# Kernel optimization log

Hardware: AMD Instinct MI355X
Metric: run time of the kernel (lower is better)

The kernel has to match this reference:

```python
import jax, jax.numpy as jnp
import numpy as np

D = 512; H = 8; HD = D // H; L = 6; QD = 16; MAXLEN = 1000

def _pos_encoding(max_len, d):
    pos = jnp.arange(max_len, dtype=jnp.float32)[:, None]
    div = jnp.exp(jnp.arange(0, d, 2, dtype=jnp.float32) * (-np.log(10000.0) / d))
    pe = jnp.zeros((max_len, d), jnp.float32)
    pe = pe.at[:, 0::2].set(jnp.sin(pos * div))
    pe = pe.at[:, 1::2].set(jnp.cos(pos * div))
    return pe

def _quantum(x, W, b, qwr, qwi, sg, em, mb):
    # QuantumInspiredLayer: classical tanh branch + quantum branch fused by sigmoid gate
    classical = jnp.tanh(x @ W + b)
    qs = x @ sg                          # (B,S,QD) real superposition amplitudes
    ev_r = qs @ qwr                      # complex evolution, real/imag parts kept separate
    ev_i = qs @ qwi
    en_r = ev_r @ em                     # entanglement (real matrix)
    en_i = ev_i @ em
    probs = en_r ** 2 + en_i ** 2        # |entangled|^2, (B,S,QD)
    qout = probs @ mb                    # measurement, (B,S,D)
    fw = jax.nn.sigmoid(jnp.mean(probs, axis=-1, keepdims=True))  # (B,S,1)
    return fw * qout + (1.0 - fw) * classical, probs

def _layer(x, p):
    (Wq, bq, Wk, bk, Wv, bv, Wo, bo,
     qW, qb, qr, qi, qsg, qem, qmb,
     kW, kb, kr, ki, ksg, kem, kmb, g, beta) = p
    B, S, _ = x.shape
    Q = x @ Wq + bq
    K = x @ Wk + bk
    Vv = x @ Wv + bv
    Qq, qp = _quantum(x, qW, qb, qr, qi, qsg, qem, qmb)
    Kq, kp = _quantum(x, kW, kb, kr, ki, ksg, kem, kmb)
    Qf = (0.7 * Q + 0.3 * Qq).reshape(B, S, H, HD).transpose(0, 2, 1, 3)  # (B,H,S,hd)
    Kf = (0.7 * K + 0.3 * Kq).reshape(B, S, H, HD).transpose(0, 2, 1, 3)
    Vh = Vv.reshape(B, S, H, HD).transpose(0, 2, 1, 3)
    scores = jnp.einsum('bhid,bhjd->bhij', Qf, Kf) / np.sqrt(HD).astype(np.float32)
    interf = jnp.einsum('biq,bjq->bij', qp, kp)   # quantum interference term (B,S,S)
    scores = scores + 0.1 * interf[:, None]       # broadcast over heads
    attn = jax.nn.softmax(scores, axis=-1)        # dropout=eval mode (identity)
    ctx = jnp.einsum('bhij,bhjd->bhid', attn, Vh).transpose(0, 2, 1, 3).reshape(B, S, D)
    y = ctx @ Wo + bo + x                         # residual, then LayerNorm
    mu = jnp.mean(y, axis=-1, keepdims=True)
    var = jnp.mean((y - mu) ** 2, axis=-1, keepdims=True)
    y = (y - mu) / jnp.sqrt(var + 1e-5) * g + beta
    return y, attn

def setup_inputs() -> dict:
    key = jax.random.key(0)
    ks = iter(jax.random.split(key, 64))
    def rn(shape, s=0.02):
        return (jax.random.normal(next(ks), shape) * s).astype(jnp.float32)
    B, S, V = 4, 512, 32000
    inp = {
        'text_input': jax.random.randint(next(ks), (B, S), 0, V),
        'visual_input': rn((B, 2048), 1.0),
        'temporal_input': rn((B, 64), 1.0),
        'embed': rn((V, D)),
        'Wvis': rn((2048, D)), 'bvis': jnp.zeros((D,), jnp.float32),
        'Wtemp': rn((64, D)), 'btemp': jnp.zeros((D,), jnp.float32),
        'Wq': rn((L, D, D)), 'bq': jnp.zeros((L, D), jnp.float32),
        'Wk': rn((L, D, D)), 'bk': jnp.zeros((L, D), jnp.float32),
        'Wv': rn((L, D, D)), 'bv': jnp.zeros((L, D), jnp.float32),
        'Wo': rn((L, D, D)), 'bo': jnp.zeros((L, D), jnp.float32),
        'qW': rn((L, D, D)), 'qb': jnp.zeros((L, D), jnp.float32),
        'q_qwr': rn((L, QD, QD), 0.05), 'q_qwi': rn((L, QD, QD), 0.05),
        'q_sg': rn((L, D, QD), 0.05), 'q_em': rn((L, QD, QD), 0.05), 'q_mb': rn((L, QD, D), 0.05),
        'kW': rn((L, D, D)), 'kb': jnp.zeros((L, D), jnp.float32),
        'k_qwr': rn((L, QD, QD), 0.05), 'k_qwi': rn((L, QD, QD), 0.05),
        'k_sg': rn((L, D, QD), 0.05), 'k_em': rn((L, QD, QD), 0.05), 'k_mb': rn((L, QD, D), 0.05),
        'ln_g': jnp.ones((L, D), jnp.float32), 'ln_b': jnp.zeros((L, D), jnp.float32),
        'Ws': rn((D, 64)), 'bs_': jnp.zeros((64,), jnp.float32),
        'Wd': rn((D, 5)), 'bd': jnp.zeros((5,), jnp.float32),
        'We': rn((D, 1)), 'be': jnp.zeros((1,), jnp.float32),
    }
    return inp

def reference(text_input, visual_input, temporal_input, embed, Wvis, bvis, Wtemp, btemp,
              Wq, bq, Wk, bk, Wv, bv, Wo, bo,
              qW, qb, q_qwr, q_qwi, q_sg, q_em, q_mb,
              kW, kb, k_qwr, k_qwi, k_sg, k_em, k_mb,
              ln_g, ln_b, Ws, bs_, Wd, bd, We, be):
    B, S = text_input.shape
    x = (embed[text_input]
         + (visual_input @ Wvis + bvis)[:, None, :]
         + (temporal_input @ Wtemp + btemp)[:, None, :])
    x = x + _pos_encoding(MAXLEN, D)[None, :S, :]
    attns = []
    for l in range(L):
        p = (Wq[l], bq[l], Wk[l], bk[l], Wv[l], bv[l], Wo[l], bo[l],
             qW[l], qb[l], q_qwr[l], q_qwi[l], q_sg[l], q_em[l], q_mb[l],
             kW[l], kb[l], k_qwr[l], k_qwi[l], k_sg[l], k_em[l], k_mb[l],
             ln_g[l], ln_b[l])
        x, a = _layer(x, p)
        attns.append(a)
    pooled = jnp.mean(x, axis=1)  # no attention_mask -> simple mean pool
    skill = jax.nn.sigmoid(pooled @ Ws + bs_)
    diff = jax.nn.softmax(pooled @ Wd + bd, axis=-1)
    eng = jax.nn.sigmoid(pooled @ We + be)
    return skill, diff, eng, x, jnp.stack(attns)
```

## Files before the change

### kernel.cpp

```cpp
#include <hip/hip_runtime.h>
#include <hip/hip_bf16.h>

typedef __attribute__((ext_vector_type(4))) float f32x4;
typedef __attribute__((ext_vector_type(8))) short s16x8;

__device__ __forceinline__ unsigned short f2b(float f) {
  unsigned int u = __float_as_uint(f);
  unsigned int r = (u + 0x7FFFu + ((u >> 16) & 1u)) >> 16;
  return (unsigned short)r;
}
__device__ __forceinline__ float b2f(unsigned short h) {
  return __uint_as_float(((unsigned int)h) << 16);
}
__device__ __forceinline__ void gload16(const void* g, void* l) {
  __builtin_amdgcn_global_load_lds(
      (const __attribute__((address_space(1))) void*)g,
      (__attribute__((address_space(3))) void*)l, 16, 0, 0);
}

enum { MODE_F32 = 0, MODE_VT = 1, MODE_Y = 2 };
struct OutSpec { void* ptr; int mode; };
struct Outs5 { OutSpec o[5]; };
struct Ptr6 { const float* p[6]; };

template<int BM, int BN, int WGM, int WGN>
__global__ __launch_bounds__(256) void gemm_nt(
    const unsigned short* __restrict__ A, int lda, long long strideA,
    const unsigned short* __restrict__ Bm, int ldb, long long strideB,
    const float* __restrict__ biasBase, int biasStride, int perZ,
    Outs5 outs, const float* __restrict__ resid, int K)
{
  constexpr int BK = 32;
  constexpr int WM = BM / WGM, WN = BN / WGN;
  constexpr int WR = WM / 16, WC = WN / 16;
  constexpr int CHA = BM * BK / 8;
  constexpr int CHB = BN * BK / 8;
  __shared__ unsigned short lds_a[2][BM * BK];
  __shared__ unsigned short lds_b[2][BN * BK];
  const int z = blockIdx.z;
  const int tid = threadIdx.x;
  const int wave = tid >> 6, lane = tid & 63;
  const int l16 = lane & 15, lhi = lane >> 4;
  const int wm = (wave / WGN) * WM, wn = (wave % WGN) * WN;
  const int m0 = blockIdx.x * BM, n0 = blockIdx.y * BN;
  const unsigned short* Ap = A + (long long)z * strideA;
  const unsigned short* Bp = Bm + (long long)z * strideB;

  auto stage = [&](int buf, int k0) {
#pragma unroll
    for (int p = 0; p < CHA / 256; ++p) {
      int t = p * 256 + tid;
      gload16(Ap + (long long)(m0 + (t >> 2)) * lda + k0 + (t & 3) * 8, &lds_a[buf][t * 8]);
    }
    if constexpr (CHA % 256) {
      if (tid < CHA % 256) {
        int t = (CHA / 256) * 256 + tid;
        gload16(Ap + (long long)(m0 + (t >> 2)) * lda + k0 + (t & 3) * 8, &lds_a[buf][t * 8]);
      }
    }
#pragma unroll
    for (int p = 0; p < CHB / 256; ++p) {
      int t = p * 256 + tid;
      gload16(Bp + (long long)(n0 + (t >> 2)) * ldb + k0 + (t & 3) * 8, &lds_b[buf][t * 8]);
    }
    if constexpr (CHB % 256) {
      if (tid < CHB % 256) {
        int t = (CHB / 256) * 256 + tid;
        gload16(Bp + (long long)(n0 + (t >> 2)) * ldb + k0 + (t & 3) * 8, &lds_b[buf][t * 8]);
      }
    }
  };

  f32x4 acc[WR][WC];
#pragma unroll
  for (int r = 0; r < WR; ++r)
#pragma unroll
    for (int c = 0; c < WC; ++c) { f32x4 zz = {0.f, 0.f, 0.f, 0.f}; acc[r][c] = zz; }

  stage(0, 0);
  __syncthreads();
  int cur = 0;
  for (int k0 = 0; k0 < K; k0 += BK) {
    if (k0 + BK < K) stage(cur ^ 1, k0 + BK);
    s16x8 af[WR], bfv[WC];
#pragma unroll
    for (int r = 0; r < WR; ++r)
      af[r] = *(const s16x8*)&lds_a[cur][(wm + r * 16 + l16) * BK + lhi * 8];
#pragma unroll
    for (int c = 0; c < WC; ++c)
      bfv[c] = *(const s16x8*)&lds_b[cur][(wn + c * 16 + l16) * BK + lhi * 8];
#pragma unroll
    for (int r = 0; r < WR; ++r)
#pragma unroll
      for (int c = 0; c < WC; ++c)
        acc[r][c] = __builtin_amdgcn_mfma_f32_16x16x32_bf16(af[r], bfv[c], acc[r][c], 0, 0, 0);
    __syncthreads();
    cur ^= 1;
  }

  OutSpec spec = perZ ? outs.o[z] : outs.o[0];
  const float* bias = biasBase ? (biasBase + (long long)z * biasStride) : nullptr;
#pragma unroll
  for (int r = 0; r < WR; ++r) {
#pragma unroll
    for (int c = 0; c < WC; ++c) {
      int n = n0 + wn + c * 16 + l16;
      int rb = m0 + wm + r * 16 + lhi * 4;
      float bv = bias ? bias[n] : 0.f;
      float vv[4];
#pragma unroll
      for (int j = 0; j < 4; ++j) vv[j] = acc[r][c][j] + bv;
      if (spec.mode == MODE_F32) {
#pragma unroll
        for (int j = 0; j < 4; ++j)
          ((float*)spec.ptr)[(long long)(rb + j) * 512 + n] = vv[j];
      } else if (spec.mode == MODE_VT) {
        int b = rb >> 9, s = rb & 511;
        ushort4 pk;
        pk.x = f2b(vv[0]); pk.y = f2b(vv[1]); pk.z = f2b(vv[2]); pk.w = f2b(vv[3]);
        *(ushort4*)&((unsigned short*)spec.ptr)[
            (((long long)(b * 8 + (n >> 6))) * 64 + (n & 63)) * 512 + s] = pk;
      } else {
#pragma unroll
        for (int j = 0; j < 4; ++j)
          ((float*)spec.ptr)[(long long)(rb + j) * 512 + n] =
              vv[j] + resid[(long long)(rb + j) * 512 + n];
      }
    }
  }
}

__global__ __launch_bounds__(256, 1) void fused_attn(
    const unsigned short* __restrict__ Qe, const unsigned short* __restrict__ Ke,
    const unsigned short* __restrict__ Vt, float* __restrict__ attn,
    unsigned short* __restrict__ ctx)
{
  __shared__ unsigned short lds[55296];
  const int z = blockIdx.x, rb = blockIdx.y;
  const int m0 = rb * 64;
  const int b = z >> 3, h = z & 7;
  const int tid = threadIdx.x;
  const int w = tid >> 6, lane = tid & 63;
  const int l16 = lane & 15, lhi = lane >> 4;
  const int rx3 = l16 & 3, rx7 = l16 & 7;

#pragma unroll
  for (int p = 0; p < 3; ++p) {
    int t = p * 256 + tid;
    int row = t / 12, c = t % 12;
    gload16(Qe + ((long long)(z * 512 + m0 + row)) * 96 + (c ^ (row & 3)) * 8, &lds[t * 8]);
  }
#pragma unroll
  for (int p = 0; p < 24; ++p) {
    int t = p * 256 + tid;
    int row = t / 12, c = t % 12;
    gload16(Ke + ((long long)(z * 512 + row)) * 96 + (c ^ (row & 3)) * 8, &lds[6144 + t * 8]);
  }
  __syncthreads();

  const unsigned short* Qs = lds;
  const unsigned short* Ks = lds + 6144;
  s16x8 aq[3];
#pragma unroll
  for (int kk = 0; kk < 3; ++kk)
    aq[kk] = *(const s16x8*)&Qs[(w * 16 + l16) * 96 + (kk * 4 + (lhi ^ rx3)) * 8];
  f32x4 acc[32];
#pragma unroll
  for (int c = 0; c < 32; ++c) { f32x4 zz = {0.f, 0.f, 0.f, 0.f}; acc[c] = zz; }
#pragma unroll
  for (int c = 0; c < 32; ++c) {
#pragma unroll
    for (int kk = 0; kk < 3; ++kk) {
      s16x8 bf = *(const s16x8*)&Ks[(c * 16 + l16) * 96 + (kk * 4 + (lhi ^ rx3)) * 8];
      acc[c] = __builtin_amdgcn_mfma_f32_16x16x32_bf16(aq[kk], bf, acc[c], 0, 0, 0);
    }
  }

  float inv[4];
#pragma unroll
  for (int j = 0; j < 4; ++j) {
    float mx = acc[0][j];
#pragma unroll
    for (int c = 1; c < 32; ++c) mx = fmaxf(mx, acc[c][j]);
    mx = fmaxf(mx, __shfl_xor(mx, 1));
    mx = fmaxf(mx, __shfl_xor(mx, 2));
    mx = fmaxf(mx, __shfl_xor(mx, 4));
    mx = fmaxf(mx, __shfl_xor(mx, 8));
    float sum = 0.f;
#pragma unroll
    for (int c = 0; c < 32; ++c) { float e = __expf(acc[c][j] - mx); acc[c][j] = e; sum += e; }
    sum += __shfl_xor(sum, 1);
    sum += __shfl_xor(sum, 2);
    sum += __shfl_xor(sum, 4);
    sum += __shfl_xor(sum, 8);
    inv[j] = 1.f / sum;
  }
  __syncthreads();

#pragma unroll
  for (int p = 0; p < 8; ++p) {
    int t = p * 256 + tid;
    int row = t >> 5, c = t & 31;
    gload16(Vt + (long long)z * 32768 + row * 512 + (c ^ (row & 7)) * 8, &lds[32768 + t * 8]);
  }
  unsigned short* S = lds;
#pragma unroll
  for (int j = 0; j < 4; ++j) {
    int row_l = w * 16 + lhi * 4 + j;
    int rs = row_l & 7;
    unsigned short* srow = S + row_l * 512;
#pragma unroll
    for (int c = 0; c < 32; ++c) {
      float p = acc[c][j] * inv[j];
      int col = c * 16 + l16;
      srow[((col >> 3) ^ rs) * 8 + (col & 7)] = f2b(p);
    }
  }
  __syncthreads();

  {
    float* ap = attn + (long long)z * 262144;
#pragma unroll
    for (int i = 0; i < 16; ++i) {
      int cid = i * 256 + tid;
      int row = cid >> 6, g = cid & 63;
      int rs = row & 7;
      s16x8 v = *(const s16x8*)&S[row * 512 + (g ^ rs) * 8];
      f32x4 o0, o1;
#pragma unroll
      for (int e = 0; e < 4; ++e) { o0[e] = b2f((unsigned short)v[e]); o1[e] = b2f((unsigned short)v[4 + e]); }
      float* dst = ap + (long long)(m0 + row) * 512 + g * 8;
      *(f32x4*)dst = o0;
      *(f32x4*)(dst + 4) = o1;
    }
  }

  const unsigned short* Vl = lds + 32768;
  f32x4 acc2[4];
#pragma unroll
  for (int c2 = 0; c2 < 4; ++c2) { f32x4 zz = {0.f, 0.f, 0.f, 0.f}; acc2[c2] = zz; }
  const int qrow = w * 16 + l16;
#pragma unroll
  for (int kk = 0; kk < 8; ++kk) {
    s16x8 a = *(const s16x8*)&S[qrow * 512 + ((kk * 4 + lhi) ^ rx7) * 8];
#pragma unroll
    for (int c2 = 0; c2 < 4; ++c2) {
      s16x8 bf = *(const s16x8*)&Vl[(c2 * 16 + l16) * 256 + ((kk * 4 + lhi) ^ rx7) * 8];
      acc2[c2] = __builtin_amdgcn_mfma_f32_16x16x32_bf16(a, bf, acc2[c2], 0, 0, 0);
    }
  }
  __syncthreads();
#pragma unroll
  for (int p = 0; p < 8; ++p) {
    int t = p * 256 + tid;
    int row = t >> 5, c = t & 31;
    gload16(Vt + (long long)z * 32768 + row * 512 + 256 + (c ^ (row & 7)) * 8,
            &lds[32768 + t * 8]);
  }
  __syncthreads();
#pragma unroll
  for (int kk = 8; kk < 16; ++kk) {
    s16x8 a = *(const s16x8*)&S[qrow * 512 + ((kk * 4 + lhi) ^ rx7) * 8];
#pragma unroll
    for (int c2 = 0; c2 < 4; ++c2) {
      s16x8 bf = *(const s16x8*)&Vl[(c2 * 16 + l16) * 256 + (((kk - 8) * 4 + lhi) ^ rx7) * 8];
      acc2[c2] = __builtin_amdgcn_mfma_f32_16x16x32_bf16(a, bf, acc2[c2], 0, 0, 0);
    }
  }
#pragma unroll
  for (int c2 = 0; c2 < 4; ++c2) {
#pragma unroll
    for (int j = 0; j < 4; ++j) {
      int row_g = m0 + w * 16 + lhi * 4 + j;
      ctx[((long long)(b * 512 + row_g)) * 512 + h * 64 + c2 * 16 + l16] = f2b(acc2[c2][j]);
    }
  }
}

__global__ __launch_bounds__(256) void wt_k(Ptr6 srcs, unsigned short* __restrict__ wt) {
  __shared__ float tile[32][33];
  int zz = blockIdx.z;
  int l = zz / 6, mat = zz % 6;
  const float* src = srcs.p[mat] + (long long)l * 262144;
  int tx = threadIdx.x, ty = threadIdx.y;
  int n0 = blockIdx.x * 32, k0 = blockIdx.y * 32;
#pragma unroll
  for (int r = 0; r < 4; ++r)
    tile[ty + r * 8][tx] = src[(long long)(k0 + ty + r * 8) * 512 + n0 + tx];
  __syncthreads();
#pragma unroll
  for (int r = 0; r < 4; ++r)
    wt[(long long)zz * 262144 + (long long)(n0 + ty + r * 8) * 512 + k0 + tx] =
        f2b(tile[tx][ty + r * 8]);
}

__global__ __launch_bounds__(256) void prep_k(Ptr6 biases,
    const float* __restrict__ qwr, const float* __restrict__ qwi, const float* __restrict__ qem,
    const float* __restrict__ kwr, const float* __restrict__ kwi, const float* __restrict__ kem,
    float* __restrict__ biasPacked, float* __restrict__ ArAi) {
  int l = blockIdx.x, t = threadIdx.x;
  for (int m = 0; m < 6; ++m)
    for (int d = t; d < 512; d += 256)
      biasPacked[(l * 6 + m) * 512 + d] = biases.p[m][l * 512 + d];
  int i = t >> 4, j = t & 15;
  const float* em0 = qem + l * 256;
  float ar = 0.f, ai = 0.f;
  for (int tt = 0; tt < 16; ++tt) {
    ar += qwr[l * 256 + i * 16 + tt] * em0[tt * 16 + j];
    ai += qwi[l * 256 + i * 16 + tt] * em0[tt * 16 + j];
  }
  ArAi[(l * 4 + 0) * 256 + t] = ar;
  ArAi[(l * 4 + 1) * 256 + t] = ai;
  const float* em1 = kem + l * 256;
  ar = 0.f; ai = 0.f;
  for (int tt = 0; tt < 16; ++tt) {
    ar += kwr[l * 256 + i * 16 + tt] * em1[tt * 16 + j];
    ai += kwi[l * 256 + i * 16 + tt] * em1[tt * 16 + j];
  }
  ArAi[(l * 4 + 2) * 256 + t] = ar;
  ArAi[(l * 4 + 3) * 256 + t] = ai;
}

__global__ __launch_bounds__(512) void vispart_k(const float* __restrict__ vis,
    const float* __restrict__ Wvis, float* __restrict__ part) {
  int b = blockIdx.x, chunk = blockIdx.y, d = threadIdx.x;
  float acc = 0.f;
  for (int k = chunk * 64; k < chunk * 64 + 64; ++k)
    acc += vis[b * 2048 + k] * Wvis[(long long)k * 512 + d];
  part[(b * 32 + chunk) * 512 + d] = acc;
}
__global__ __launch_bounds__(512) void projsum_k(const float* __restrict__ part,
    const float* __restrict__ bvis, const float* __restrict__ temporal,
    const float* __restrict__ Wtemp, const float* __restrict__ btemp, float* __restrict__ proj) {
  int b = blockIdx.x, d = threadIdx.x;
  float acc = bvis[d] + btemp[d];
  for (int c = 0; c < 32; ++c) acc += part[(b * 32 + c) * 512 + d];
  for (int k = 0; k < 64; ++k) acc += temporal[b * 64 + k] * Wtemp[k * 512 + d];
  proj[b * 512 + d] = acc;
}

__global__ __launch_bounds__(512) void embed_k(const int* __restrict__ text,
    const float* __restrict__ emb, const float* __restrict__ proj,
    float* __restrict__ x, unsigned short* __restrict__ xb) {
  int row = blockIdx.x;
  int b = row >> 9, s = row & 511;
  int d = threadIdx.x;
  int tok = text[row];
  float v = emb[(long long)tok * 512 + d] + proj[b * 512 + d];
  float fr = __expf((float)((d >> 1) << 1) * (-9.2103403719761836f / 512.f));
  float ang = (float)s * fr;
  v += (d & 1) ? cosf(ang) : sinf(ang);
  x[(long long)row * 512 + d] = v;
  xb[(long long)row * 512 + d] = f2b(v);
}

__global__ __launch_bounds__(64) void quantum_k(const float* __restrict__ x,
    const float* __restrict__ sg_q, const float* __restrict__ sg_k,
    const float* __restrict__ ArAiL, float* __restrict__ qp, float* __restrict__ kp,
    float* __restrict__ fwq, float* __restrict__ fwk) {
  int row = blockIdx.x, side = blockIdx.y, lane = threadIdx.x;
  const float* sg = side ? sg_k : sg_q;
  const float* Ar = ArAiL + side * 512;
  const float* Ai = Ar + 256;
  float acc[16];
#pragma unroll
  for (int j = 0; j < 16; ++j) acc[j] = 0.f;
  const float* xr = x + (long long)row * 512;
#pragma unroll
  for (int kk = 0; kk < 8; ++kk) {
    float xv = xr[kk * 64 + lane];
    const float* sgr = sg + (kk * 64 + lane) * 16;
#pragma unroll
    for (int j = 0; j < 16; ++j) acc[j] += xv * sgr[j];
  }
#pragma unroll
  for (int s = 32; s; s >>= 1)
#pragma unroll
    for (int j = 0; j < 16; ++j) acc[j] += __shfl_xor(acc[j], s);
  int j = lane & 15;
  float tr = 0.f, ti = 0.f;
#pragma unroll
  for (int t = 0; t < 16; ++t) {
    tr += acc[t] * Ar[t * 16 + j];
    ti += acc[t] * Ai[t * 16 + j];
  }
  float p = tr * tr + ti * ti;
  float ps = p;
#pragma unroll
  for (int s = 1; s < 16; s <<= 1) ps += __shfl_xor(ps, s);
  if (lane < 16) (side ? kp : qp)[row * 16 + lane] = p;
  if (lane == 0) (side ? fwk : fwq)[row] = 1.f / (1.f + __expf(-ps * (1.f / 16.f)));
}

struct FuseP {
  const float* lin; const float* cl; const float* qp; const float* fw;
  const float* mb; unsigned short* ext; float sA, sB;
};
struct Fuse2 { FuseP s[2]; };
__global__ __launch_bounds__(512) void fuse_k(Fuse2 fp) {
  FuseP P = fp.s[blockIdx.y];
  int row = blockIdx.x;
  int b = row >> 9, i = row & 511;
  int d = threadIdx.x;
  const float* qpr = P.qp + row * 16;
  float fwv = P.fw[row];
  float qout = 0.f;
#pragma unroll
  for (int t = 0; t < 16; ++t) qout += qpr[t] * P.mb[t * 512 + d];
  float qq = fwv * qout + (1.f - fwv) * tanhf(P.cl[(long long)row * 512 + d]);
  float val = (0.7f * P.lin[(long long)row * 512 + d] + 0.3f * qq) * P.sA;
  int h = d >> 6, dd = d & 63;
  P.ext[(((long long)(b * 8 + h)) * 512 + i) * 96 + dd] = f2b(val);
  if (d < 128) {
    int h2 = d >> 4, j = d & 15;
    P.ext[(((long long)(b * 8 + h2)) * 512 + i) * 96 + 64 + j] = f2b(P.sB * qpr[j]);
  } else if (d < 256) {
    int t2 = d - 128;
    int h2 = t2 >> 4, j = t2 & 15;
    P.ext[(((long long)(b * 8 + h2)) * 512 + i) * 96 + 80 + j] = 0;
  }
}

__global__ __launch_bounds__(256) void ln_k(const float* __restrict__ y,
    const float* __restrict__ g, const float* __restrict__ be,
    float* __restrict__ xo, unsigned short* __restrict__ xb, float* __restrict__ xo2) {
  int wv = threadIdx.x >> 6, lane = threadIdx.x & 63;
  long long row = (long long)blockIdx.x * 4 + wv;
  const float* yr = y + row * 512 + lane * 8;
  f32x4 a = *(const f32x4*)yr, b = *(const f32x4*)(yr + 4);
  float s = a[0] + a[1] + a[2] + a[3] + b[0] + b[1] + b[2] + b[3];
#pragma unroll
  for (int m = 32; m; m >>= 1) s += __shfl_xor(s, m);
  float mu = s * (1.f / 512.f);
  float d[8], vs = 0.f;
#pragma unroll
  for (int j = 0; j < 4; ++j) { d[j] = a[j] - mu; vs += d[j] * d[j]; }
#pragma unroll
  for (int j = 0; j < 4; ++j) { d[4 + j] = b[j] - mu; vs += d[4 + j] * d[4 + j]; }
#pragma unroll
  for (int m = 32; m; m >>= 1) vs += __shfl_xor(vs, m);
  float rstd = rsqrtf(vs * (1.f / 512.f) + 1e-5f);
  f32x4 g0 = *(const f32x4*)(g + lane * 8), g1 = *(const f32x4*)(g + lane * 8 + 4);
  f32x4 b0 = *(const f32x4*)(be + lane * 8), b1 = *(const f32x4*)(be + lane * 8 + 4);
  f32x4 o0, o1; s16x8 ob;
#pragma unroll
  for (int j = 0; j < 4; ++j) { o0[j] = d[j] * rstd * g0[j] + b0[j]; ob[j] = (short)f2b(o0[j]); }
#pragma unroll
  for (int j = 0; j < 4; ++j) { o1[j] = d[4 + j] * rstd * g1[j] + b1[j]; ob[4 + j] = (short)f2b(o1[j]); }
  float* xr = xo + row * 512 + lane * 8;
  *(f32x4*)xr = o0; *(f32x4*)(xr + 4) = o1;
  *(s16x8*)(xb + row * 512 + lane * 8) = ob;
  if (xo2) {
    float* x2 = xo2 + row * 512 + lane * 8;
    *(f32x4*)x2 = o0; *(f32x4*)(x2 + 4) = o1;
  }
}

__global__ __launch_bounds__(512) void poolpart_k(const float* __restrict__ x,
                                                   float* __restrict__ part) {
  int b = blockIdx.x, ch = blockIdx.y, d = threadIdx.x;
  float s = 0.f;
  for (int r = 0; r < 64; ++r) s += x[((long long)(b * 512 + ch * 64 + r)) * 512 + d];
  part[(b * 8 + ch) * 512 + d] = s;
}
__global__ __launch_bounds__(512) void head_k(const float* __restrict__ part,
    const float* __restrict__ Ws, const float* __restrict__ bs,
    const float* __restrict__ Wd, const float* __restrict__ bd,
    const float* __restrict__ We, const float* __restrict__ be, float* __restrict__ out) {
  __shared__ float pooled[512];
  __shared__ float dl[5];
  int b = blockIdx.x, d = threadIdx.x;
  float s = 0.f;
  for (int t = 0; t < 8; ++t) s += part[(b * 8 + t) * 512 + d];
  pooled[d] = s * (1.f / 512.f);
  __syncthreads();
  {
    int o = d >> 3, sub = d & 7;
    float a = 0.f;
    for (int t = sub; t < 512; t += 8) a += pooled[t] * Ws[t * 64 + o];
    a += __shfl_xor(a, 1); a += __shfl_xor(a, 2); a += __shfl_xor(a, 4);
    if (sub == 0) out[b * 64 + o] = 1.f / (1.f + __expf(-(a + bs[o])));
  }
  if (d < 40) {
    int o = d >> 3, sub = d & 7;
    float a = 0.f;
    for (int t = sub; t < 512; t += 8) a += pooled[t] * Wd[t * 5 + o];
    a += __shfl_xor(a, 1); a += __shfl_xor(a, 2); a += __shfl_xor(a, 4);
    if (sub == 0) dl[o] = a + bd[o];
  } else if (d >= 64 && d < 72) {
    int sub = d & 7;
    float a = 0.f;
    for (int t = sub; t < 512; t += 8) a += pooled[t] * We[t];
    a += __shfl_xor(a, 1); a += __shfl_xor(a, 2); a += __shfl_xor(a, 4);
    if (sub == 0) out[276 + b] = 1.f / (1.f + __expf(-(a + be[0])));
  }
  __syncthreads();
  if (d < 5) {
    float mx = dl[0];
    for (int j = 1; j < 5; ++j) mx = fmaxf(mx, dl[j]);
    float sm = 0.f;
    for (int j = 0; j < 5; ++j) sm += __expf(dl[j] - mx);
    out[256 + b * 5 + d] = __expf(dl[d] - mx) / sm;
  }
}

extern "C" void kernel_launch(void* const* d_in, const int* in_sizes, int n_in,
                              void* d_out, int out_size, void* d_ws, size_t ws_size,
                              hipStream_t stream) {
  (void)in_sizes; (void)n_in; (void)out_size; (void)ws_size;
  const int*   text     = (const int*)  d_in[0];
  const float* visual   = (const float*)d_in[1];
  const float* temporal = (const float*)d_in[2];
  const float* embedw   = (const float*)d_in[3];
  const float* Wvis  = (const float*)d_in[4];  const float* bvis  = (const float*)d_in[5];
  const float* Wtemp = (const float*)d_in[6];  const float* btemp = (const float*)d_in[7];
  const float* Wq = (const float*)d_in[8];   const float* bq = (const float*)d_in[9];
  const float* Wk = (const float*)d_in[10];  const float* bk = (const float*)d_in[11];
  const float* Wv = (const float*)d_in[12];  const float* bv = (const float*)d_in[13];
  const float* Wo = (const float*)d_in[14];  const float* bo = (const float*)d_in[15];
  const float* qW = (const float*)d_in[16];  const float* qb = (const float*)d_in[17];
  const float* q_qwr = (const float*)d_in[18]; const float* q_qwi = (const float*)d_in[19];
  const float* q_sg  = (const float*)d_in[20]; const float* q_em  = (const float*)d_in[21];
  const float* q_mb  = (const float*)d_in[22];
  const float* kW = (const float*)d_in[23];  const float* kb = (const float*)d_in[24];
  const float* k_qwr = (const float*)d_in[25]; const float* k_qwi = (const float*)d_in[26];
  const float* k_sg  = (const float*)d_in[27]; const float* k_em  = (const float*)d_in[28];
  const float* k_mb  = (const float*)d_in[29];
  const float* ln_g = (const float*)d_in[30]; const float* ln_b = (const float*)d_in[31];
  const float* Ws = (const float*)d_in[32];  const float* bs_ = (const float*)d_in[33];
  const float* Wd = (const float*)d_in[34];  const float* bd = (const float*)d_in[35];
  const float* We = (const float*)d_in[36];  const float* be = (const float*)d_in[37];
  float* out = (float*)d_out;

  char* w = (char*)d_ws;
  auto alloc = [&](size_t bytes) {
    char* p = w;
    w += (bytes + 255) & ~(size_t)255;
    return p;
  };
  float* ws_x   = (float*)alloc(2048ll * 512 * 4);
  unsigned short* ws_xb = (unsigned short*)alloc(2048ll * 512 * 2);
  unsigned short* ws_Wt = (unsigned short*)alloc(36ll * 262144 * 2);
  float* ws_bias = (float*)alloc(6ll * 6 * 512 * 4);
  float* ws_ArAi = (float*)alloc(6ll * 1024 * 4);
  float* ws_proj = (float*)alloc(4ll * 512 * 4);
  float* ws_vp   = (float*)alloc(4ll * 32 * 512 * 4);
  float* ws_Q    = (float*)alloc(2048ll * 512 * 4);
  float* ws_K    = (float*)alloc(2048ll * 512 * 4);
  float* ws_Cq   = (float*)alloc(2048ll * 512 * 4);
  float* ws_Ck   = (float*)alloc(2048ll * 512 * 4);
  float* ws_qp   = (float*)alloc(2048ll * 16 * 4);
  float* ws_kp   = (float*)alloc(2048ll * 16 * 4);
  float* ws_fwq  = (float*)alloc(2048ll * 4);
  float* ws_fwk  = (float*)alloc(2048ll * 4);
  unsigned short* ws_Vt   = (unsigned short*)alloc(2048ll * 512 * 2);
  unsigned short* ws_Qext = (unsigned short*)alloc(4ll * 8 * 512 * 96 * 2);
  unsigned short* ws_Kext = (unsigned short*)alloc(4ll * 8 * 512 * 96 * 2);
  unsigned short* ws_ctx  = (unsigned short*)alloc(2048ll * 512 * 2);
  float* ws_y    = (float*)alloc(2048ll * 512 * 4);

  Ptr6 wsrc = {{Wq, Wk, Wv, qW, kW, Wo}};
  wt_k<<<dim3(16, 16, 36), dim3(32, 8), 0, stream>>>(wsrc, ws_Wt);
  Ptr6 bsrc = {{bq, bk, bv, qb, kb, bo}};
  prep_k<<<dim3(6), dim3(256), 0, stream>>>(bsrc, q_qwr, q_qwi, q_em, k_qwr, k_qwi, k_em,
                                            ws_bias, ws_ArAi);
  vispart_k<<<dim3(4, 32), dim3(512), 0, stream>>>(visual, Wvis, ws_vp);
  projsum_k<<<dim3(4), dim3(512), 0, stream>>>(ws_vp, bvis, temporal, Wtemp, btemp, ws_proj);
  embed_k<<<dim3(2048), dim3(512), 0, stream>>>(text, embedw, ws_proj, ws_x, ws_xb);

  const long long ATTN_OFF = 280ll + 1048576ll;
  for (int l = 0; l < 6; ++l) {
    const unsigned short* WtL = ws_Wt + (long long)l * 6 * 262144;
    const float* biasL = ws_bias + (long long)l * 6 * 512;

    Outs5 o5{};
    o5.o[0] = { ws_Q, MODE_F32 };  o5.o[1] = { ws_K, MODE_F32 };
    o5.o[2] = { ws_Vt, MODE_VT };  o5.o[3] = { ws_Cq, MODE_F32 };
    o5.o[4] = { ws_Ck, MODE_F32 };
    gemm_nt<128, 128, 2, 2><<<dim3(16, 4, 5), 256, 0, stream>>>(
        ws_xb, 512, 0ll, WtL, 512, 262144ll, biasL, 512, 1, o5, nullptr, 512);

    quantum_k<<<dim3(2048, 2), 64, 0, stream>>>(ws_x, q_sg + l * 8192, k_sg + l * 8192,
        ws_ArAi + l * 1024, ws_qp, ws_kp, ws_fwq, ws_fwk);

    Fuse2 f2{};
    f2.s[0] = { ws_Q, ws_Cq, ws_qp, ws_fwq, q_mb + l * 8192, ws_Qext, 0.125f, 0.1f };
    f2.s[1] = { ws_K, ws_Ck, ws_kp, ws_fwk, k_mb + l * 8192, ws_Kext, 1.0f, 1.0f };
    fuse_k<<<dim3(2048, 2), dim3(512), 0, stream>>>(f2);

    fused_attn<<<dim3(32, 8), 256, 0, stream>>>(
        ws_Qext, ws_Kext, ws_Vt, out + ATTN_OFF + (long long)l * 8388608, ws_ctx);

    Outs5 oy{};
    oy.o[0] = { ws_y, MODE_Y };
    gemm_nt<64, 64, 2, 2><<<dim3(32, 8, 1), 256, 0, stream>>>(
        ws_ctx, 512, 0ll, WtL + 5 * 262144, 512, 0ll, biasL + 5 * 512, 0, 0, oy, ws_x, 512);

    ln_k<<<dim3(512), dim3(256), 0, stream>>>(ws_y, ln_g + l * 512, ln_b + l * 512,
        ws_x, ws_xb, (l == 5) ? (out + 280) : nullptr);
  }

  poolpart_k<<<dim3(4, 8), dim3(512), 0, stream>>>(ws_x, ws_vp);
  head_k<<<dim3(4), dim3(512), 0, stream>>>(ws_vp, Ws, bs_, Wd, bd, We, be, out);
}
```

Measured before the change: 521.9 us.

## Fuse output projection GEMM with residual LayerNorm and mean-pool partials

Replaces the Wo GEMM, the separate LayerNorm kernel and the pooling kernel with one kernel. Each block computes full 32-row by 512-column output tiles, adds bias and residual into LDS, normalizes rows in place and, on the last layer, writes per-block pooled partial sums. This removes the fp32 y round trip through global memory and two launches per layer. The cost is only 64 blocks on a large GPU, each block loading the whole Wo weight matrix, and heavy LDS use that lowers occupancy.

```diff
diff --git a/kernel.cpp b/kernel.cpp
--- a/kernel.cpp
+++ b/kernel.cpp
@@ -18,7 +18,7 @@
       (__attribute__((address_space(3))) void*)l, 16, 0, 0);
 }
 
-enum { MODE_F32 = 0, MODE_VT = 1, MODE_Y = 2 };
+enum { MODE_F32 = 0, MODE_VT = 1 };
 struct OutSpec { void* ptr; int mode; };
 struct Outs5 { OutSpec o[5]; };
 struct Ptr6 { const float* p[6]; };
@@ -28,7 +28,7 @@
     const unsigned short* __restrict__ A, int lda, long long strideA,
     const unsigned short* __restrict__ Bm, int ldb, long long strideB,
     const float* __restrict__ biasBase, int biasStride, int perZ,
-    Outs5 outs, const float* __restrict__ resid, int K)
+    Outs5 outs, int K)
 {
   constexpr int BK = 32;
   constexpr int WM = BM / WGM, WN = BN / WGN;
@@ -114,19 +114,142 @@
 #pragma unroll
         for (int j = 0; j < 4; ++j)
           ((float*)spec.ptr)[(long long)(rb + j) * 512 + n] = vv[j];
-      } else if (spec.mode == MODE_VT) {
+      } else {
         int b = rb >> 9, s = rb & 511;
         ushort4 pk;
         pk.x = f2b(vv[0]); pk.y = f2b(vv[1]); pk.z = f2b(vv[2]); pk.w = f2b(vv[3]);
         *(ushort4*)&((unsigned short*)spec.ptr)[
             (((long long)(b * 8 + (n >> 6))) * 64 + (n & 63)) * 512 + s] = pk;
-      } else {
-#pragma unroll
-        for (int j = 0; j < 4; ++j)
-          ((float*)spec.ptr)[(long long)(rb + j) * 512 + n] =
-              vv[j] + resid[(long long)(rb + j) * 512 + n];
       }
     }
+  }
+}
+
+__global__ __launch_bounds__(256) void ygemm_ln(
+    const unsigned short* __restrict__ ctx, const unsigned short* __restrict__ WoT,
+    const float* __restrict__ bias, const float* __restrict__ g, const float* __restrict__ be,
+    float* __restrict__ x, unsigned short* __restrict__ xb,
+    float* __restrict__ xo2, float* __restrict__ pool)
+{
+  __shared__ char smem[77824];
+  unsigned short* lds_a = (unsigned short*)smem;
+  unsigned short* lds_b = (unsigned short*)(smem + 4096);
+  float* ylds = (float*)smem;
+  float* wpart = (float*)(smem + 69632);
+  const int tid = threadIdx.x;
+  const int w = tid >> 6, lane = tid & 63;
+  const int l16 = lane & 15, lhi = lane >> 4;
+  const int m0 = blockIdx.x * 32;
+  const int wn = w * 128;
+
+  auto stage = [&](int buf, int k0) {
+    if (tid < 128) {
+      int row = tid >> 2, cg = tid & 3;
+      gload16(ctx + (long long)(m0 + row) * 512 + k0 + cg * 8, lds_a + buf * 1024 + tid * 8);
+    }
+#pragma unroll
+    for (int p = 0; p < 8; ++p) {
+      int t = p * 256 + tid;
+      int row = t >> 2, cg = t & 3;
+      gload16(WoT + (long long)row * 512 + k0 + cg * 8, lds_b + buf * 16384 + t * 8);
+    }
+  };
+
+  f32x4 acc[2][8];
+#pragma unroll
+  for (int r = 0; r < 2; ++r)
+#pragma unroll
+    for (int c = 0; c < 8; ++c) { f32x4 zz = {0.f, 0.f, 0.f, 0.f}; acc[r][c] = zz; }
+
+  stage(0, 0);
+  __syncthreads();
+  int cur = 0;
+  for (int k0 = 0; k0 < 512; k0 += 32) {
+    if (k0 + 32 < 512) stage(cur ^ 1, k0 + 32);
+    s16x8 af[2], bfv[8];
+#pragma unroll
+    for (int r = 0; r < 2; ++r)
+      af[r] = *(const s16x8*)&lds_a[cur * 1024 + (r * 16 + l16) * 32 + lhi * 8];
+#pragma unroll
+    for (int c = 0; c < 8; ++c)
+      bfv[c] = *(const s16x8*)&lds_b[cur * 16384 + (wn + c * 16 + l16) * 32 + lhi * 8];
+#pragma unroll
+    for (int r = 0; r < 2; ++r)
+#pragma unroll
+      for (int c = 0; c < 8; ++c)
+        acc[r][c] = __builtin_amdgcn_mfma_f32_16x16x32_bf16(af[r], bfv[c], acc[r][c], 0, 0, 0);
+    __syncthreads();
+    cur ^= 1;
+  }
+
+#pragma unroll
+  for (int r = 0; r < 2; ++r) {
+#pragma unroll
+    for (int c = 0; c < 8; ++c) {
+      int col = wn + c * 16 + l16;
+      int rb = r * 16 + lhi * 4;
+      float bv = bias[col];
+#pragma unroll
+      for (int j = 0; j < 4; ++j) {
+        int row = rb + j;
+        ylds[row * 520 + col] = acc[r][c][j] + bv + x[(long long)(m0 + row) * 512 + col];
+      }
+    }
+  }
+  __syncthreads();
+
+  f32x4 g0 = *(const f32x4*)(g + lane * 8), g1 = *(const f32x4*)(g + lane * 8 + 4);
+  f32x4 b0 = *(const f32x4*)(be + lane * 8), b1 = *(const f32x4*)(be + lane * 8 + 4);
+  float psum[8];
+#pragma unroll
+  for (int e = 0; e < 8; ++e) psum[e] = 0.f;
+#pragma unroll
+  for (int i = 0; i < 8; ++i) {
+    int row = w + i * 4;
+    const float* yr = ylds + row * 520 + lane * 8;
+    f32x4 a = *(const f32x4*)yr, bq = *(const f32x4*)(yr + 4);
+    float s = a[0] + a[1] + a[2] + a[3] + bq[0] + bq[1] + bq[2] + bq[3];
+#pragma unroll
+    for (int m = 32; m; m >>= 1) s += __shfl_xor(s, m);
+    float mu = s * (1.f / 512.f);
+    float d[8], vs = 0.f;
+#pragma unroll
+    for (int j = 0; j < 4; ++j) { d[j] = a[j] - mu; vs += d[j] * d[j]; }
+#pragma unroll
+    for (int j = 0; j < 4; ++j) { d[4 + j] = bq[j] - mu; vs += d[4 + j] * d[4 + j]; }
+#pragma unroll
+    for (int m = 32; m; m >>= 1) vs += __shfl_xor(vs, m);
+    float rstd = rsqrtf(vs * (1.f / 512.f) + 1e-5f);
+    f32x4 o0, o1; s16x8 ob;
+#pragma unroll
+    for (int j = 0; j < 4; ++j) { o0[j] = d[j] * rstd * g0[j] + b0[j]; ob[j] = (short)f2b(o0[j]); }
+#pragma unroll
+    for (int j = 0; j < 4; ++j) { o1[j] = d[4 + j] * rstd * g1[j] + b1[j]; ob[4 + j] = (short)f2b(o1[j]); }
+    long long gro = (long long)(m0 + row) * 512 + lane * 8;
+    *(f32x4*)(x + gro) = o0; *(f32x4*)(x + gro + 4) = o1;
+    *(s16x8*)(xb + gro) = ob;
+    if (xo2) { *(f32x4*)(xo2 + gro) = o0; *(f32x4*)(xo2 + gro + 4) = o1; }
+    if (pool) {
+#pragma unroll
+      for (int e = 0; e < 4; ++e) { psum[e] += o0[e]; psum[4 + e] += o1[e]; }
+    }
+  }
+  if (pool) {
+    f32x4 p0, p1;
+#pragma unroll
+    for (int e = 0; e < 4; ++e) { p0[e] = psum[e]; p1[e] = psum[4 + e]; }
+    *(f32x4*)(wpart + w * 512 + lane * 8) = p0;
+    *(f32x4*)(wpart + w * 512 + lane * 8 + 4) = p1;
+    __syncthreads();
+    float s0 = 0.f, s1 = 0.f;
+#pragma unroll
+    for (int w2 = 0; w2 < 4; ++w2) {
+      s0 += wpart[w2 * 512 + tid];
+      s1 += wpart[w2 * 512 + 256 + tid];
+    }
+    long long po = (long long)((m0 >> 9) * 16 + (blockIdx.x & 15)) * 512;
+    pool[po + tid] = s0;
+    pool[po + 256 + tid] = s1;
   }
 }
 
@@ -223,13 +346,13 @@
 #pragma unroll
     for (int i = 0; i < 16; ++i) {
       int cid = i * 256 + tid;
-      int row = cid >> 6, g = cid & 63;
+      int row = cid >> 6, gch = cid & 63;
       int rs = row & 7;
-      s16x8 v = *(const s16x8*)&S[row * 512 + (g ^ rs) * 8];
+      s16x8 v = *(const s16x8*)&S[row * 512 + (gch ^ rs) * 8];
       f32x4 o0, o1;
 #pragma unroll
       for (int e = 0; e < 4; ++e) { o0[e] = b2f((unsigned short)v[e]); o1[e] = b2f((unsigned short)v[4 + e]); }
-      float* dst = ap + (long long)(m0 + row) * 512 + g * 8;
+      float* dst = ap + (long long)(m0 + row) * 512 + gch * 8;
       *(f32x4*)dst = o0;
       *(f32x4*)(dst + 4) = o1;
     }
@@ -421,48 +544,6 @@
   }
 }
 
-__global__ __launch_bounds__(256) void ln_k(const float* __restrict__ y,
-    const float* __restrict__ g, const float* __restrict__ be,
-    float* __restrict__ xo, unsigned short* __restrict__ xb, float* __restrict__ xo2) {
-  int wv = threadIdx.x >> 6, lane = threadIdx.x & 63;
-  long long row = (long long)blockIdx.x * 4 + wv;
-  const float* yr = y + row * 512 + lane * 8;
-  f32x4 a = *(const f32x4*)yr, b = *(const f32x4*)(yr + 4);
-  float s = a[0] + a[1] + a[2] + a[3] + b[0] + b[1] + b[2] + b[3];
-#pragma unroll
-  for (int m = 32; m; m >>= 1) s += __shfl_xor(s, m);
-  float mu = s * (1.f / 512.f);
-  float d[8], vs = 0.f;
-#pragma unroll
-  for (int j = 0; j < 4; ++j) { d[j] = a[j] - mu; vs += d[j] * d[j]; }
-#pragma unroll
-  for (int j = 0; j < 4; ++j) { d[4 + j] = b[j] - mu; vs += d[4 + j] * d[4 + j]; }
-#pragma unroll
-  for (int m = 32; m; m >>= 1) vs += __shfl_xor(vs, m);
-  float rstd = rsqrtf(vs * (1.f / 512.f) + 1e-5f);
-  f32x4 g0 = *(const f32x4*)(g + lane * 8), g1 = *(const f32x4*)(g + lane * 8 + 4);
-  f32x4 b0 = *(const f32x4*)(be + lane * 8), b1 = *(const f32x4*)(be + lane * 8 + 4);
-  f32x4 o0, o1; s16x8 ob;
-#pragma unroll
-  for (int j = 0; j < 4; ++j) { o0[j] = d[j] * rstd * g0[j] + b0[j]; ob[j] = (short)f2b(o0[j]); }
-#pragma unroll
-  for (int j = 0; j < 4; ++j) { o1[j] = d[4 + j] * rstd * g1[j] + b1[j]; ob[4 + j] = (short)f2b(o1[j]); }
-  float* xr = xo + row * 512 + lane * 8;
-  *(f32x4*)xr = o0; *(f32x4*)(xr + 4) = o1;
-  *(s16x8*)(xb + row * 512 + lane * 8) = ob;
-  if (xo2) {
-    float* x2 = xo2 + row * 512 + lane * 8;
-    *(f32x4*)x2 = o0; *(f32x4*)(x2 + 4) = o1;
-  }
-}
-
-__global__ __launch_bounds__(512) void poolpart_k(const float* __restrict__ x,
-                                                   float* __restrict__ part) {
-  int b = blockIdx.x, ch = blockIdx.y, d = threadIdx.x;
-  float s = 0.f;
-  for (int r = 0; r < 64; ++r) s += x[((long long)(b * 512 + ch * 64 + r)) * 512 + d];
-  part[(b * 8 + ch) * 512 + d] = s;
-}
 __global__ __launch_bounds__(512) void head_k(const float* __restrict__ part,
     const float* __restrict__ Ws, const float* __restrict__ bs,
     const float* __restrict__ Wd, const float* __restrict__ bd,
@@ -471,7 +552,7 @@
   __shared__ float dl[5];
   int b = blockIdx.x, d = threadIdx.x;
   float s = 0.f;
-  for (int t = 0; t < 8; ++t) s += part[(b * 8 + t) * 512 + d];
+  for (int t = 0; t < 16; ++t) s += part[(b * 16 + t) * 512 + d];
   pooled[d] = s * (1.f / 512.f);
   __syncthreads();
   {
@@ -557,7 +638,6 @@
   unsigned short* ws_Qext = (unsigned short*)alloc(4ll * 8 * 512 * 96 * 2);
   unsigned short* ws_Kext = (unsigned short*)alloc(4ll * 8 * 512 * 96 * 2);
   unsigned short* ws_ctx  = (unsigned short*)alloc(2048ll * 512 * 2);
-  float* ws_y    = (float*)alloc(2048ll * 512 * 4);
 
   Ptr6 wsrc = {{Wq, Wk, Wv, qW, kW, Wo}};
   wt_k<<<dim3(16, 16, 36), dim3(32, 8), 0, stream>>>(wsrc, ws_Wt);
@@ -578,7 +658,7 @@
     o5.o[2] = { ws_Vt, MODE_VT };  o5.o[3] = { ws_Cq, MODE_F32 };
     o5.o[4] = { ws_Ck, MODE_F32 };
     gemm_nt<128, 128, 2, 2><<<dim3(16, 4, 5), 256, 0, stream>>>(
-        ws_xb, 512, 0ll, WtL, 512, 262144ll, biasL, 512, 1, o5, nullptr, 512);
+        ws_xb, 512, 0ll, WtL, 512, 262144ll, biasL, 512, 1, o5, 512);
 
     quantum_k<<<dim3(2048, 2), 64, 0, stream>>>(ws_x, q_sg + l * 8192, k_sg + l * 8192,
         ws_ArAi + l * 1024, ws_qp, ws_kp, ws_fwq, ws_fwk);
@@ -591,15 +671,11 @@
     fused_attn<<<dim3(32, 8), 256, 0, stream>>>(
         ws_Qext, ws_Kext, ws_Vt, out + ATTN_OFF + (long long)l * 8388608, ws_ctx);
 
-    Outs5 oy{};
-    oy.o[0] = { ws_y, MODE_Y };
-    gemm_nt<64, 64, 2, 2><<<dim3(32, 8, 1), 256, 0, stream>>>(
-        ws_ctx, 512, 0ll, WtL + 5 * 262144, 512, 0ll, biasL + 5 * 512, 0, 0, oy, ws_x, 512);
-
-    ln_k<<<dim3(512), dim3(256), 0, stream>>>(ws_y, ln_g + l * 512, ln_b + l * 512,
-        ws_x, ws_xb, (l == 5) ? (out + 280) : nullptr);
-  }
-
-  poolpart_k<<<dim3(4, 8), dim3(512), 0, stream>>>(ws_x, ws_vp);
+    ygemm_ln<<<dim3(64), dim3(256), 0, stream>>>(
+        ws_ctx, WtL + 5 * 262144, biasL + 5 * 512,
+        ln_g + l * 512, ln_b + l * 512, ws_x, ws_xb,
+        (l == 5) ? (out + 280) : nullptr, (l == 5) ? ws_vp : nullptr);
+  }
+
   head_k<<<dim3(4), dim3(512), 0, stream>>>(ws_vp, Ws, bs_, Wd, bd, We, be, out);
 }
```

Result: slower. 541.8 us (+3.8%).

## Fuse QKV and quantum GEMMs with gating epilogue into one kernel

Applied to the files above, without the earlier changes.

Replaces the five-output projection GEMM plus separate fuse kernel with a single kernel. Each block computes the linear and classical-branch GEMMs together, runs the quantum measurement matmul on MFMA, and writes the bf16 Q/K extended tensors and V transpose directly, which removes the fp32 Q/K/Cq/Ck intermediates and their global round trips. Attention-probability output is also written straight from registers instead of being staged through LDS and re-read, dropping a barrier. In exchange the new GEMM uses smaller tiles with no LDS swizzle, converts probs to bf16 for the measurement product, and writes the ext tensors with scattered stores.

```diff
diff --git a/kernel.cpp b/kernel.cpp
--- a/kernel.cpp
+++ b/kernel.cpp
@@ -130,6 +130,165 @@
   }
 }
 
+__global__ __launch_bounds__(256) void qkv_fuse(
+    const unsigned short* __restrict__ xb, const unsigned short* __restrict__ Wt,
+    const float* __restrict__ biasP,
+    const float* __restrict__ qp, const float* __restrict__ kp,
+    const float* __restrict__ fwq, const float* __restrict__ fwk,
+    const unsigned short* __restrict__ mbT,
+    unsigned short* __restrict__ Qext, unsigned short* __restrict__ Kext,
+    unsigned short* __restrict__ Vt)
+{
+  __shared__ unsigned short lds[2][8192];
+  const int z = blockIdx.z;
+  const int tid = threadIdx.x;
+  const int wave = tid >> 6, lane = tid & 63;
+  const int l16 = lane & 15, lhi = lane >> 4;
+  const int wm = (wave >> 1) * 64, wn = (wave & 1) * 32;
+  const int m0 = blockIdx.x * 128, n0 = blockIdx.y * 64;
+  const int mat1 = z;
+  const unsigned short* B1p = Wt + (long long)mat1 * 262144;
+  const unsigned short* B2p = Wt + (long long)(z + 3) * 262144;
+
+  auto stage = [&](int buf, int k0) {
+#pragma unroll
+    for (int p = 0; p < 2; ++p) {
+      int t = p * 256 + tid;
+      gload16(xb + (long long)(m0 + (t >> 2)) * 512 + k0 + (t & 3) * 8, &lds[buf][t * 8]);
+    }
+    {
+      int row = tid >> 2, cg = tid & 3;
+      gload16(B1p + (long long)(n0 + row) * 512 + k0 + cg * 8, &lds[buf][4096 + tid * 8]);
+      if (z < 2)
+        gload16(B2p + (long long)(n0 + row) * 512 + k0 + cg * 8, &lds[buf][6144 + tid * 8]);
+    }
+  };
+
+  f32x4 acc1[4][2], acc2[4][2];
+#pragma unroll
+  for (int r = 0; r < 4; ++r)
+#pragma unroll
+    for (int c = 0; c < 2; ++c) {
+      f32x4 zz = {0.f, 0.f, 0.f, 0.f};
+      acc1[r][c] = zz; acc2[r][c] = zz;
+    }
+
+  stage(0, 0);
+  __syncthreads();
+  int cur = 0;
+  for (int k0 = 0; k0 < 512; k0 += 32) {
+    if (k0 + 32 < 512) stage(cur ^ 1, k0 + 32);
+    s16x8 af[4], b1f[2], b2f[2];
+#pragma unroll
+    for (int r = 0; r < 4; ++r)
+      af[r] = *(const s16x8*)&lds[cur][(wm + r * 16 + l16) * 32 + lhi * 8];
+#pragma unroll
+    for (int c = 0; c < 2; ++c) {
+      b1f[c] = *(const s16x8*)&lds[cur][4096 + (wn + c * 16 + l16) * 32 + lhi * 8];
+      b2f[c] = *(const s16x8*)&lds[cur][6144 + (wn + c * 16 + l16) * 32 + lhi * 8];
+    }
+#pragma unroll
+    for (int r = 0; r < 4; ++r)
+#pragma unroll
+      for (int c = 0; c < 2; ++c)
+        acc1[r][c] = __builtin_amdgcn_mfma_f32_16x16x32_bf16(af[r], b1f[c], acc1[r][c], 0, 0, 0);
+    if (z < 2) {
+#pragma unroll
+      for (int r = 0; r < 4; ++r)
+#pragma unroll
+        for (int c = 0; c < 2; ++c)
+          acc2[r][c] = __builtin_amdgcn_mfma_f32_16x16x32_bf16(af[r], b2f[c], acc2[r][c], 0, 0, 0);
+    }
+    __syncthreads();
+    cur ^= 1;
+  }
+
+  const float* bias1 = biasP + mat1 * 512;
+  if (z == 2) {
+#pragma unroll
+    for (int r = 0; r < 4; ++r)
+#pragma unroll
+      for (int c = 0; c < 2; ++c) {
+        int n = n0 + wn + c * 16 + l16;
+        int rb = m0 + wm + r * 16 + lhi * 4;
+        float bv = bias1[n];
+        int bb = rb >> 9, s = rb & 511;
+        ushort4 pk;
+        pk.x = f2b(acc1[r][c][0] + bv); pk.y = f2b(acc1[r][c][1] + bv);
+        pk.z = f2b(acc1[r][c][2] + bv); pk.w = f2b(acc1[r][c][3] + bv);
+        *(ushort4*)&Vt[(((long long)(bb * 8 + (n >> 6))) * 64 + (n & 63)) * 512 + s] = pk;
+      }
+    return;
+  }
+
+  const float* probs = z ? kp : qp;
+  const float* fw    = z ? fwk : fwq;
+  unsigned short* ext = z ? Kext : Qext;
+  const unsigned short* mbs = mbT + z * 16384;
+  const float* bias2 = biasP + (z + 3) * 512;
+  const float sA = z ? 1.0f : 0.125f;
+  const float sB = z ? 1.0f : 0.1f;
+
+  s16x8 pf[4];
+#pragma unroll
+  for (int r = 0; r < 4; ++r) {
+    s16x8 v = {0, 0, 0, 0, 0, 0, 0, 0};
+    if (lhi < 2) {
+      const float* pr = probs + (m0 + wm + r * 16 + l16) * 16 + lhi * 8;
+#pragma unroll
+      for (int e = 0; e < 8; ++e) v[e] = (short)f2b(pr[e]);
+    }
+    pf[r] = v;
+  }
+  s16x8 mf[2];
+#pragma unroll
+  for (int c = 0; c < 2; ++c)
+    mf[c] = *(const s16x8*)&mbs[(n0 + wn + c * 16 + l16) * 32 + lhi * 8];
+  f32x4 qo[4][2];
+#pragma unroll
+  for (int r = 0; r < 4; ++r)
+#pragma unroll
+    for (int c = 0; c < 2; ++c) {
+      f32x4 zz = {0.f, 0.f, 0.f, 0.f};
+      qo[r][c] = __builtin_amdgcn_mfma_f32_16x16x32_bf16(pf[r], mf[c], zz, 0, 0, 0);
+    }
+
+#pragma unroll
+  for (int r = 0; r < 4; ++r) {
+    int rb = m0 + wm + r * 16 + lhi * 4;
+    float fwj[4];
+#pragma unroll
+    for (int j = 0; j < 4; ++j) fwj[j] = fw[rb + j];
+#pragma unroll
+    for (int c = 0; c < 2; ++c) {
+      int n = n0 + wn + c * 16 + l16;
+      float b1 = bias1[n], b2 = bias2[n];
+      int h = n >> 6, dd = n & 63;
+#pragma unroll
+      for (int j = 0; j < 4; ++j) {
+        int row = rb + j;
+        int bb = row >> 9, ii = row & 511;
+        float lin = acc1[r][c][j] + b1;
+        float cl  = acc2[r][c][j] + b2;
+        float qq = fwj[j] * qo[r][c][j] + (1.f - fwj[j]) * tanhf(cl);
+        ext[(((long long)(bb * 8 + h)) * 512 + ii) * 96 + dd] = f2b((0.7f * lin + 0.3f * qq) * sA);
+      }
+    }
+  }
+
+  if (blockIdx.y == 0) {
+    for (int t = tid; t < 128 * 256; t += 256) {
+      int row_l = t >> 8;
+      int rem = t & 255;
+      int h2 = rem >> 5, e = rem & 31;
+      int row = m0 + row_l;
+      int bb = row >> 9, ii = row & 511;
+      unsigned short v = (e < 16) ? f2b(sB * probs[row * 16 + e]) : (unsigned short)0;
+      ext[(((long long)(bb * 8 + h2)) * 512 + ii) * 96 + 64 + e] = v;
+    }
+  }
+}
+
 __global__ __launch_bounds__(256, 1) void fused_attn(
     const unsigned short* __restrict__ Qe, const unsigned short* __restrict__ Ke,
     const unsigned short* __restrict__ Vt, float* __restrict__ attn,
@@ -204,36 +363,24 @@
     gload16(Vt + (long long)z * 32768 + row * 512 + (c ^ (row & 7)) * 8, &lds[32768 + t * 8]);
   }
   unsigned short* S = lds;
-#pragma unroll
-  for (int j = 0; j < 4; ++j) {
-    int row_l = w * 16 + lhi * 4 + j;
-    int rs = row_l & 7;
-    unsigned short* srow = S + row_l * 512;
-#pragma unroll
-    for (int c = 0; c < 32; ++c) {
-      float p = acc[c][j] * inv[j];
-      int col = c * 16 + l16;
-      srow[((col >> 3) ^ rs) * 8 + (col & 7)] = f2b(p);
-    }
-  }
-  __syncthreads();
-
   {
     float* ap = attn + (long long)z * 262144;
 #pragma unroll
-    for (int i = 0; i < 16; ++i) {
-      int cid = i * 256 + tid;
-      int row = cid >> 6, g = cid & 63;
-      int rs = row & 7;
-      s16x8 v = *(const s16x8*)&S[row * 512 + (g ^ rs) * 8];
-      f32x4 o0, o1;
-#pragma unroll
-      for (int e = 0; e < 4; ++e) { o0[e] = b2f((unsigned short)v[e]); o1[e] = b2f((unsigned short)v[4 + e]); }
-      float* dst = ap + (long long)(m0 + row) * 512 + g * 8;
-      *(f32x4*)dst = o0;
-      *(f32x4*)(dst + 4) = o1;
-    }
-  }
+    for (int j = 0; j < 4; ++j) {
+      int row_l = w * 16 + lhi * 4 + j;
+      int rs = row_l & 7;
+      float* arow = ap + (long long)(m0 + row_l) * 512;
+      unsigned short* srow = S + row_l * 512;
+#pragma unroll
+      for (int c = 0; c < 32; ++c) {
+        float p = acc[c][j] * inv[j];
+        int col = c * 16 + l16;
+        arow[col] = p;
+        srow[((col >> 3) ^ rs) * 8 + (col & 7)] = f2b(p);
+      }
+    }
+  }
+  __syncthreads();
 
   const unsigned short* Vl = lds + 32768;
   f32x4 acc2[4];
@@ -297,7 +444,9 @@
 __global__ __launch_bounds__(256) void prep_k(Ptr6 biases,
     const float* __restrict__ qwr, const float* __restrict__ qwi, const float* __restrict__ qem,
     const float* __restrict__ kwr, const float* __restrict__ kwi, const float* __restrict__ kem,
-    float* __restrict__ biasPacked, float* __restrict__ ArAi) {
+    const float* __restrict__ qmb, const float* __restrict__ kmb,
+    float* __restrict__ biasPacked, float* __restrict__ ArAi,
+    unsigned short* __restrict__ mbT) {
   int l = blockIdx.x, t = threadIdx.x;
   for (int m = 0; m < 6; ++m)
     for (int d = t; d < 512; d += 256)
@@ -319,6 +468,18 @@
   }
   ArAi[(l * 4 + 2) * 256 + t] = ar;
   ArAi[(l * 4 + 3) * 256 + t] = ai;
+  for (int n = t; n < 512; n += 256) {
+#pragma unroll
+    for (int k = 0; k < 16; ++k) {
+      mbT[(long long)(l * 2 + 0) * 16384 + n * 32 + k] = f2b(qmb[l * 8192 + k * 512 + n]);
+      mbT[(long long)(l * 2 + 1) * 16384 + n * 32 + k] = f2b(kmb[l * 8192 + k * 512 + n]);
+    }
+#pragma unroll
+    for (int k = 16; k < 32; ++k) {
+      mbT[(long long)(l * 2 + 0) * 16384 + n * 32 + k] = 0;
+      mbT[(long long)(l * 2 + 1) * 16384 + n * 32 + k] = 0;
+    }
+  }
 }
 
 __global__ __launch_bounds__(512) void vispart_k(const float* __restrict__ vis,
@@ -390,35 +551,6 @@
   for (int s = 1; s < 16; s <<= 1) ps += __shfl_xor(ps, s);
   if (lane < 16) (side ? kp : qp)[row * 16 + lane] = p;
   if (lane == 0) (side ? fwk : fwq)[row] = 1.f / (1.f + __expf(-ps * (1.f / 16.f)));
-}
-
-struct FuseP {
-  const float* lin; const float* cl; const float* qp; const float* fw;
-  const float* mb; unsigned short* ext; float sA, sB;
-};
-struct Fuse2 { FuseP s[2]; };
-__global__ __launch_bounds__(512) void fuse_k(Fuse2 fp) {
-  FuseP P = fp.s[blockIdx.y];
-  int row = blockIdx.x;
-  int b = row >> 9, i = row & 511;
-  int d = threadIdx.x;
-  const float* qpr = P.qp + row * 16;
-  float fwv = P.fw[row];
-  float qout = 0.f;
-#pragma unroll
-  for (int t = 0; t < 16; ++t) qout += qpr[t] * P.mb[t * 512 + d];
-  float qq = fwv * qout + (1.f - fwv) * tanhf(P.cl[(long long)row * 512 + d]);
-  float val = (0.7f * P.lin[(long long)row * 512 + d] + 0.3f * qq) * P.sA;
-  int h = d >> 6, dd = d & 63;
-  P.ext[(((long long)(b * 8 + h)) * 512 + i) * 96 + dd] = f2b(val);
-  if (d < 128) {
-    int h2 = d >> 4, j = d & 15;
-    P.ext[(((long long)(b * 8 + h2)) * 512 + i) * 96 + 64 + j] = f2b(P.sB * qpr[j]);
-  } else if (d < 256) {
-    int t2 = d - 128;
-    int h2 = t2 >> 4, j = t2 & 15;
-    P.ext[(((long long)(b * 8 + h2)) * 512 + i) * 96 + 80 + j] = 0;
-  }
 }
 
 __global__ __launch_bounds__(256) void ln_k(const float* __restrict__ y,
@@ -543,12 +675,9 @@
   unsigned short* ws_Wt = (unsigned short*)alloc(36ll * 262144 * 2);
   float* ws_bias = (float*)alloc(6ll * 6 * 512 * 4);
   float* ws_ArAi = (float*)alloc(6ll * 1024 * 4);
+  unsigned short* ws_mbT = (unsigned short*)alloc(12ll * 16384 * 2);
   float* ws_proj = (float*)alloc(4ll * 512 * 4);
   float* ws_vp   = (float*)alloc(4ll * 32 * 512 * 4);
-  float* ws_Q    = (float*)alloc(2048ll * 512 * 4);
-  float* ws_K    = (float*)alloc(2048ll * 512 * 4);
-  float* ws_Cq   = (float*)alloc(2048ll * 512 * 4);
-  float* ws_Ck   = (float*)alloc(2048ll * 512 * 4);
   float* ws_qp   = (float*)alloc(2048ll * 16 * 4);
   float* ws_kp   = (float*)alloc(2048ll * 16 * 4);
   float* ws_fwq  = (float*)alloc(2048ll * 4);
@@ -563,7 +692,7 @@
   wt_k<<<dim3(16, 16, 36), dim3(32, 8), 0, stream>>>(wsrc, ws_Wt);
   Ptr6 bsrc = {{bq, bk, bv, qb, kb, bo}};
   prep_k<<<dim3(6), dim3(256), 0, stream>>>(bsrc, q_qwr, q_qwi, q_em, k_qwr, k_qwi, k_em,
-                                            ws_bias, ws_ArAi);
+                                            q_mb, k_mb, ws_bias, ws_ArAi, ws_mbT);
   vispart_k<<<dim3(4, 32), dim3(512), 0, stream>>>(visual, Wvis, ws_vp);
   projsum_k<<<dim3(4), dim3(512), 0, stream>>>(ws_vp, bvis, temporal, Wtemp, btemp, ws_proj);
   embed_k<<<dim3(2048), dim3(512), 0, stream>>>(text, embedw, ws_proj, ws_x, ws_xb);
@@ -573,20 +702,12 @@
     const unsigned short* WtL = ws_Wt + (long long)l * 6 * 262144;
     const float* biasL = ws_bias + (long long)l * 6 * 512;
 
-    Outs5 o5{};
-    o5.o[0] = { ws_Q, MODE_F32 };  o5.o[1] = { ws_K, MODE_F32 };
-    o5.o[2] = { ws_Vt, MODE_VT };  o5.o[3] = { ws_Cq, MODE_F32 };
-    o5.o[4] = { ws_Ck, MODE_F32 };
-    gemm_nt<128, 128, 2, 2><<<dim3(16, 4, 5), 256, 0, stream>>>(
-        ws_xb, 512, 0ll, WtL, 512, 262144ll, biasL, 512, 1, o5, nullptr, 512);
-
     quantum_k<<<dim3(2048, 2), 64, 0, stream>>>(ws_x, q_sg + l * 8192, k_sg + l * 8192,
         ws_ArAi + l * 1024, ws_qp, ws_kp, ws_fwq, ws_fwk);
 
-    Fuse2 f2{};
-    f2.s[0] = { ws_Q, ws_Cq, ws_qp, ws_fwq, q_mb + l * 8192, ws_Qext, 0.125f, 0.1f };
-    f2.s[1] = { ws_K, ws_Ck, ws_kp, ws_fwk, k_mb + l * 8192, ws_Kext, 1.0f, 1.0f };
-    fuse_k<<<dim3(2048, 2), dim3(512), 0, stream>>>(f2);
+    qkv_fuse<<<dim3(16, 8, 3), 256, 0, stream>>>(
+        ws_xb, WtL, biasL, ws_qp, ws_kp, ws_fwq, ws_fwk,
+        ws_mbT + (long long)l * 32768, ws_Qext, ws_Kext, ws_Vt);
 
     fused_attn<<<dim3(32, 8), 256, 0, stream>>>(
         ws_Qext, ws_Kext, ws_Vt, out + ATTN_OFF + (long long)l * 8388608, ws_ctx);
```

After: 579.0 us. 1.11x slower.
